# Performance work log

Hardware: AMD Instinct MI355X
Metric: run time of the kernel (lower is better)

## Reference

```python
import jax, jax.numpy as jnp
import numpy as np

N_KERNELS = 11

def _kernel_mus(n):
    l = [1.0]
    bs = 2.0 / (n - 1)
    l.append(1 - bs / 2)
    for i in range(1, n - 1):
        l.append(l[i] - bs)
    return l

def _kernel_sigmas(n):
    bs = 2.0 / (n - 1)
    return [0.001] + [0.5 * bs] * (n - 1)

MU = jnp.asarray(_kernel_mus(N_KERNELS), jnp.float32)      # [K]
SIGMA = jnp.asarray(_kernel_sigmas(N_KERNELS), jnp.float32)  # [K]


def setup_inputs() -> dict:
    key = jax.random.key(0)
    ks = jax.random.split(key, 10)
    V, E, C = 50000, 300, 128
    B, Q, D = 128, 30, 200
    inp = {
        'query_tokens': jax.random.randint(ks[0], (B, Q), 0, V),
        'document_tokens': jax.random.randint(ks[1], (B, D), 0, V),
        'embedding': jax.random.normal(ks[2], (V, E), jnp.float32) * 0.1,
        'conv_w1': jax.random.normal(ks[3], (C, E, 1), jnp.float32) * 0.05,
        'conv_w2': jax.random.normal(ks[4], (C, E, 2), jnp.float32) * 0.05,
        'conv_w3': jax.random.normal(ks[5], (C, E, 3), jnp.float32) * 0.05,
        'conv_b1': jax.random.normal(ks[6], (C,), jnp.float32) * 0.01,
        'conv_b2': jax.random.normal(ks[7], (C,), jnp.float32) * 0.01,
        'conv_b3': jax.random.normal(ks[8], (C,), jnp.float32) * 0.01,
        'dense_w': jax.random.uniform(ks[9], (1, N_KERNELS * 9), jnp.float32, -0.014, 0.014),
    }
    return inp


def _conv_ngram(x_ble, w, b):
    # x_ble: [B, L, E]; w: [C, E, k]; pad (0, k-1) on the length dim -> same length out
    x = x_ble.transpose(0, 2, 1)  # [B, E, L]
    y = jax.lax.conv_general_dilated(
        x, w, window_strides=(1,), padding=[(0, w.shape[2] - 1)],
        dimension_numbers=('NCH', 'OIH', 'NCH'))
    return jax.nn.relu(y + b[None, :, None]).transpose(0, 2, 1)  # [B, L, C]


def _kernel_pool(q, d, qd_mask, q_mask):
    # q: [B,Q,C], d: [B,D,C]; cosine sim -> Gaussian RBF soft-binning -> masked log-sum pooling
    qn = q / (jnp.linalg.norm(q, axis=-1, keepdims=True) + 1e-13)
    dn = d / (jnp.linalg.norm(d, axis=-1, keepdims=True) + 1e-13)
    cos = jnp.einsum('bqc,bdc->bqd', qn, dn) * qd_mask           # [B,Q,D]
    diff = cos[..., None] - MU                                    # [B,Q,D,K]
    kern = jnp.exp(-(diff * diff) / (2.0 * SIGMA * SIGMA)) * qd_mask[..., None]
    per_kernel_query = jnp.sum(kern, axis=2)                      # [B,Q,K]
    logk = jnp.log(jnp.clip(per_kernel_query, 1e-10)) * 0.01
    return jnp.sum(logk * q_mask[..., None], axis=1)              # [B,K]


def reference(query_tokens, document_tokens, embedding,
              conv_w1, conv_w2, conv_w3, conv_b1, conv_b2, conv_b3, dense_w):
    q_mask = (query_tokens > 0).astype(jnp.float32)               # [B,Q]
    d_mask = (document_tokens > 0).astype(jnp.float32)            # [B,D]
    qd_mask = q_mask[:, :, None] * d_mask[:, None, :]             # [B,Q,D]

    q_emb = embedding[query_tokens]                               # [B,Q,E]
    d_emb = embedding[document_tokens]                            # [B,D,E]

    convs = [(conv_w1, conv_b1), (conv_w2, conv_b2), (conv_w3, conv_b3)]
    q_grams = [_conv_ngram(q_emb, w, b) for w, b in convs]
    d_grams = [_conv_ngram(d_emb, w, b) for w, b in convs]

    feats = jnp.concatenate(
        [_kernel_pool(q, d, qd_mask, q_mask) for q in q_grams for d in d_grams],
        axis=1)                                                   # [B, K*9]
    return (feats @ dense_w.T)[:, 0]                              # [B]
```

## Files before the change

### kernel.cpp

```cpp
#include <hip/hip_runtime.h>
#include <hip/hip_bf16.h>
#include <math.h>

#define B_   128
#define Qn   30
#define Dn   200
#define En   300

typedef __attribute__((ext_vector_type(8))) short short8;
typedef __attribute__((ext_vector_type(4))) float floatx4;
typedef unsigned int u32;
typedef unsigned short u16;

static __device__ __forceinline__ u16 f2b(float x) {
    union { float f; u32 u; } v; v.f = x;
    u32 r = v.u + 0x7FFFu + ((v.u >> 16) & 1u);
    return (u16)(r >> 16);
}
static __device__ __forceinline__ float bits2f(u32 u) {
    union { u32 u2; float f; } v; v.u2 = u; return v.f;
}

__global__ void prep_kernel(
    const float* __restrict__ w1, const float* __restrict__ w2, const float* __restrict__ w3,
    u16* __restrict__ Wt3)
{
    int p = (blockIdx.x*128 + blockIdx.y)*256 + threadIdx.x;
    if (p >= 245760) return;
    int ks = p / 24576;
    int r  = p - ks*24576;
    int g, rr;
    if (r < 4096)        { g = 0; rr = r;         }
    else if (r < 12288)  { g = 1; rr = r - 4096;  }
    else                 { g = 2; rr = r - 12288; }
    int j  = rr >> 12;
    int r2 = rr & 4095;
    int nt  = r2 >> 9;
    int q4  = (r2 >> 7) & 3;
    int c16 = (r2 >> 3) & 15;
    int k8  = r2 & 7;
    int ch = nt*16 + c16;
    int e  = ks*32 + q4*8 + k8;
    float v = 0.f;
    if (e < En) {
        if (g == 0)      v = w1[ch*En + e];
        else if (g == 1) v = w2[(ch*En + e)*2 + j];
        else             v = w3[(ch*En + e)*3 + j];
    }
    Wt3[p] = f2b(v);
}

__global__ __launch_bounds__(512, 4) void conv_kernel(
    const int* __restrict__ qtok, const int* __restrict__ dtok,
    const float* __restrict__ emb,
    const u16* __restrict__ Wt3,
    const float* __restrict__ b1, const float* __restrict__ b2, const float* __restrict__ b3,
    u16* __restrict__ qg, u16* __restrict__ dg,
    float* __restrict__ invnq, float* __restrict__ invnd)
{
    __shared__ __align__(16) char smem[43560];
    char* As  = smem;
    int*  toks = (int*)(smem + 43296);

    const int tile = blockIdx.x;
    const int tid = threadIdx.x;
    const int wv = tid >> 6, lane = tid & 63;
    const int l15 = lane & 15, qd4 = lane >> 4;
    const int mh = wv >> 2, nh = wv & 3;
    const int gR0 = tile*64;

    if (tid < 66) {
        int gr = gR0 + tid;
        int t = -1;
        if (gr < 32768) {
            int b = gr >> 8, pos = gr & 255;
            if (pos < Dn) t = dtok[b*Dn + pos];
            else if (pos >= 208 && pos < 238) t = qtok[b*Qn + (pos - 208)];
        }
        toks[tid] = t;
    }
    __syncthreads();

    #pragma unroll
    for (int i = 0; i < 6; ++i) {
        int idx = tid + i*512;
        if (idx < 2640) {
            int r = idx / 40, c4 = idx - r*40;
            int t = toks[r];
            u16 o0=0,o1=0,o2=0,o3=0;
            if (t >= 0) {
                float4 v = *(const float4*)(emb + t*En + c4*4);
                o0=f2b(v.x); o1=f2b(v.y); o2=f2b(v.z); o3=f2b(v.w);
            }
            u16* pdst = (u16*)(As + r*656 + c4*8);
            pdst[0]=o0; pdst[1]=o1; pdst[2]=o2; pdst[3]=o3;
        }
    }

    float bias[3][2];
    #pragma unroll
    for (int nt = 0; nt < 2; ++nt) {
        int ch = nh*32 + nt*16 + l15;
        bias[0][nt] = b1[ch];
        bias[1][nt] = b2[ch];
        bias[2][nt] = b3[ch];
    }

    floatx4 acc[3][2][2];
    #pragma unroll
    for (int g = 0; g < 3; ++g)
        #pragma unroll
        for (int mt = 0; mt < 2; ++mt)
            #pragma unroll
            for (int nt = 0; nt < 2; ++nt)
                acc[g][mt][nt] = (floatx4){0.f,0.f,0.f,0.f};

    __syncthreads();

    float4 hf[6];
    #pragma unroll
    for (int i = 0; i < 6; ++i) {
        int idx = tid + i*512;
        const float* p = emb;
        if (idx < 2640) {
            int r = idx / 40, c = idx - r*40;
            int t = toks[r];
            if (t >= 0 && c < 35) p = emb + t*En + (40 + c)*4;
        }
        hf[i] = *(const float4*)p;
    }

    #pragma unroll 1
    for (int ks = 0; ks < 5; ++ks) {
        short8 af[2][3];
        #pragma unroll
        for (int mt = 0; mt < 2; ++mt)
            #pragma unroll
            for (int j = 0; j < 3; ++j)
                af[mt][j] = *(const short8*)(As + (mh*32 + mt*16 + l15 + j)*656 + ks*64 + qd4*16);
        const u16* Wks = Wt3 + ks*24576;
        #pragma unroll
        for (int g = 0; g < 3; ++g) {
            const int cbW = (g == 0) ? 0 : (g == 1) ? 4096 : 12288;
            #pragma unroll
            for (int j = 0; j <= g; ++j) {
                const u16* bb = Wks + cbW + (j*8 + nh*2)*512 + lane*8;
                short8 w0  = *(const short8*)(bb);
                short8 w1v = *(const short8*)(bb + 512);
                #pragma unroll
                for (int mt = 0; mt < 2; ++mt) {
                    acc[g][mt][0] = __builtin_amdgcn_mfma_f32_16x16x32_bf16(
                        af[mt][j], w0,  acc[g][mt][0], 0, 0, 0);
                    acc[g][mt][1] = __builtin_amdgcn_mfma_f32_16x16x32_bf16(
                        af[mt][j], w1v, acc[g][mt][1], 0, 0, 0);
                }
            }
        }
    }

    #pragma unroll
    for (int i = 0; i < 6; ++i) {
        int idx = tid + i*512;
        if (idx < 2640) {
            int r = idx / 40, c = idx - r*40;
            int t = toks[r];
            bool ok = (t >= 0) && (c < 35);
            u16 o0=0,o1=0,o2=0,o3=0;
            if (ok) { o0=f2b(hf[i].x); o1=f2b(hf[i].y); o2=f2b(hf[i].z); o3=f2b(hf[i].w); }
            u16* pdst = (u16*)(As + r*656 + (40 + c)*8);
            pdst[0]=o0; pdst[1]=o1; pdst[2]=o2; pdst[3]=o3;
        }
    }
    __syncthreads();

    #pragma unroll 1
    for (int ks = 5; ks < 10; ++ks) {
        short8 af[2][3];
        #pragma unroll
        for (int mt = 0; mt < 2; ++mt)
            #pragma unroll
            for (int j = 0; j < 3; ++j)
                af[mt][j] = *(const short8*)(As + (mh*32 + mt*16 + l15 + j)*656 + ks*64 + qd4*16);
        const u16* Wks = Wt3 + ks*24576;
        #pragma unroll
        for (int g = 0; g < 3; ++g) {
            const int cbW = (g == 0) ? 0 : (g == 1) ? 4096 : 12288;
            #pragma unroll
            for (int j = 0; j <= g; ++j) {
                const u16* bb = Wks + cbW + (j*8 + nh*2)*512 + lane*8;
                short8 w0  = *(const short8*)(bb);
                short8 w1v = *(const short8*)(bb + 512);
                #pragma unroll
                for (int mt = 0; mt < 2; ++mt) {
                    acc[g][mt][0] = __builtin_amdgcn_mfma_f32_16x16x32_bf16(
                        af[mt][j], w0,  acc[g][mt][0], 0, 0, 0);
                    acc[g][mt][1] = __builtin_amdgcn_mfma_f32_16x16x32_bf16(
                        af[mt][j], w1v, acc[g][mt][1], 0, 0, 0);
                }
            }
        }
    }

    u16* Gs = (u16*)smem;
    #pragma unroll
    for (int g = 0; g < 3; ++g) {
        __syncthreads();
        #pragma unroll
        for (int mt = 0; mt < 2; ++mt)
            #pragma unroll
            for (int nt = 0; nt < 2; ++nt) {
                int ch = nh*32 + nt*16 + l15;
                #pragma unroll
                for (int i = 0; i < 4; ++i) {
                    int row = mh*32 + mt*16 + qd4*4 + i;
                    Gs[row*136 + ch] = f2b(fmaxf(acc[g][mt][nt][i] + bias[g][nt], 0.f));
                }
            }
        __syncthreads();

        {
            int r = tid >> 3, pp = tid & 7;
            const char* rp = (const char*)Gs + r*272 + pp*32;
            float ssum = 0.f;
            #pragma unroll
            for (int t2 = 0; t2 < 2; ++t2) {
                uint4 u = *(const uint4*)(rp + t2*16);
                float x;
                x = bits2f(u.x << 16); ssum += x*x;  x = bits2f(u.x & 0xffff0000u); ssum += x*x;
                x = bits2f(u.y << 16); ssum += x*x;  x = bits2f(u.y & 0xffff0000u); ssum += x*x;
                x = bits2f(u.z << 16); ssum += x*x;  x = bits2f(u.z & 0xffff0000u); ssum += x*x;
                x = bits2f(u.w << 16); ssum += x*x;  x = bits2f(u.w & 0xffff0000u); ssum += x*x;
            }
            ssum += __shfl_xor(ssum, 1);
            ssum += __shfl_xor(ssum, 2);
            ssum += __shfl_xor(ssum, 4);
            if (pp == 0) {
                float inv = 1.f / (sqrtf(ssum) + 1e-13f);
                int gr = gR0 + r;
                int b = gr >> 8, pos = gr & 255;
                if (pos < 208)      invnd[(g*B_ + b)*208 + pos] = inv;
                else if (pos < 238) invnq[(g*B_ + b)*32 + (pos - 208)] = inv;
            }
        }
        #pragma unroll
        for (int i = 0; i < 2; ++i) {
            int idx = tid + i*512;
            int r = idx >> 4, c16 = idx & 15;
            uint4 v = *(const uint4*)((const char*)Gs + r*272 + c16*16);
            int gr = gR0 + r;
            int b = gr >> 8, pos = gr & 255;
            if (pos < 208)      *(uint4*)(dg + ((g*B_ + b)*208 + pos)*128 + c16*8) = v;
            else if (pos < 238) *(uint4*)(qg + ((g*B_ + b)*32 + (pos - 208))*128 + c16*8) = v;
        }
    }
}

__global__ __launch_bounds__(1024, 2) void pool_kernel(
    const u16* __restrict__ qg, const u16* __restrict__ dg,
    const float* __restrict__ invnq, const float* __restrict__ invnd,
    const int* __restrict__ qtok, const int* __restrict__ dtok,
    float* __restrict__ feats)
{
    __shared__ __align__(16) u16 dsb[208*136];
    __shared__ float pk[96*12];
    __shared__ float invqA[96];
    __shared__ float qmA[96];
    __shared__ __align__(16) float invd[208];

    const int tid = threadIdx.x;
    const int b = blockIdx.y, dj = blockIdx.x;
    const int wv = tid >> 6, lane = tid & 63;
    const int l15 = lane & 15, qd4 = lane >> 4;

    for (int idx = tid; idx < 208*16; idx += 1024) {
        int r = idx >> 4, ch = idx & 15;
        uint4 v = make_uint4(0u,0u,0u,0u);
        if (r < Dn) v = *(const uint4*)(dg + ((dj*B_ + b)*208 + r)*128 + ch*8);
        *(uint4*)((char*)dsb + r*272 + ch*16) = v;
    }
    if (tid < 208) {
        float v = invnd[(dj*B_ + b)*208 + tid];
        bool ok = (tid < Dn) && (dtok[b*Dn + tid] > 0);
        invd[tid] = ok ? v : (-fabsf(v) - 1.0f);
    }
    if (tid < 96) {
        int qi = tid >> 5, qr = tid & 31;
        float v = invnq[(qi*B_ + b)*32 + qr];
        bool ok = (qr < Qn) && (qtok[b*Qn + qr] > 0);
        invqA[tid] = ok ? v : 0.f;
        qmA[tid] = ok ? 1.f : 0.f;
    }
    for (int i = tid; i < 96*12; i += 1024) pk[i] = 0.f;
    __syncthreads();

    const float CkR[9] = {8886110.5f, 162754.79f, 2980.958f, 54.598150f, 1.0f,
                          0.018315639f, 3.3546263e-4f, 6.1442124e-6f, 1.1253517e-7f};

    if (wv < 13) {
        const int t = wv;
        short8 af[4];
        #pragma unroll
        for (int ks = 0; ks < 4; ++ks)
            af[ks] = *(const short8*)((const char*)dsb + (t*16 + l15)*272 + ks*64 + qd4*16);
        floatx4 iv4 = *(const floatx4*)(invd + t*16 + qd4*4);

        #pragma unroll 1
        for (int qi = 0; qi < 3; ++qi) {
            short8 qf[2][4];
            float vq[2];
            #pragma unroll
            for (int qt = 0; qt < 2; ++qt) {
                vq[qt] = invqA[qi*32 + qt*16 + l15];
                #pragma unroll
                for (int ks = 0; ks < 4; ++ks)
                    qf[qt][ks] = *(const short8*)(qg + ((qi*B_ + b)*32 + qt*16 + l15)*128 + ks*32 + qd4*8);
            }
            floatx4 acc[2];
            acc[0] = (floatx4){0.f,0.f,0.f,0.f};
            acc[1] = (floatx4){0.f,0.f,0.f,0.f};
            #pragma unroll
            for (int ks = 0; ks < 4; ++ks)
                #pragma unroll
                for (int qt = 0; qt < 2; ++qt)
                    acc[qt] = __builtin_amdgcn_mfma_f32_16x16x32_bf16(af[ks], qf[qt][ks], acc[qt], 0, 0, 0);

            float pkl[2][11];
            #pragma unroll
            for (int qt = 0; qt < 2; ++qt)
                #pragma unroll
                for (int k = 0; k < 11; ++k) pkl[qt][k] = 0.f;

            #pragma unroll
            for (int qt = 0; qt < 2; ++qt)
                #pragma unroll
                for (int i = 0; i < 4; ++i) {
                    float cs = acc[qt][i] * vq[qt] * iv4[i];
                    cs = (cs > 0.f) ? cs : 2.0f;
                    float t0 = cs - 1.0f;
                    float u  = cs - 0.9f;
                    float s0 = __expf(-500000.f * t0 * t0);
                    float e  = __expf(-50.f * u * u);
                    float rr = __expf(-20.f * cs);
                    pkl[qt][0] += s0;
                    pkl[qt][1] += e;
                    #pragma unroll
                    for (int kk = 0; kk < 9; ++kk) {
                        e = e * rr * CkR[kk];
                        pkl[qt][2 + kk] += e;
                    }
                }
            #pragma unroll
            for (int qt = 0; qt < 2; ++qt)
                #pragma unroll
                for (int k = 0; k < 11; ++k) {
                    float v = pkl[qt][k];
                    v += __shfl_xor(v, 16);
                    v += __shfl_xor(v, 32);
                    if (qd4 == 0) atomicAdd(&pk[(qi*32 + qt*16 + l15)*12 + k], v);
                }
        }
    }
    __syncthreads();

    if (tid < 33) {
        int qi = tid / 11, k = tid - qi*11;
        float s = 0.f;
        for (int q = 0; q < Qn; ++q)
            s += qmA[qi*32 + q] * 0.01f * __logf(fmaxf(pk[(qi*32 + q)*12 + k], 1e-10f));
        feats[(b*9 + qi*3 + dj)*11 + k] = s;
    }
}

__global__ void final_kernel(const float* __restrict__ feats,
                             const float* __restrict__ dw,
                             float* __restrict__ out) {
    int b = threadIdx.x;
    if (b < B_) {
        float s = 0.f;
        for (int f = 0; f < 99; ++f) s += feats[b*99 + f] * dw[f];
        out[b] = s;
    }
}

extern "C" void kernel_launch(void* const* d_in, const int* in_sizes, int n_in,
                              void* d_out, int out_size, void* d_ws, size_t ws_size,
                              hipStream_t stream) {
    const int*   qtok = (const int*)d_in[0];
    const int*   dtok = (const int*)d_in[1];
    const float* emb  = (const float*)d_in[2];
    const float* w1   = (const float*)d_in[3];
    const float* w2   = (const float*)d_in[4];
    const float* w3   = (const float*)d_in[5];
    const float* b1   = (const float*)d_in[6];
    const float* b2   = (const float*)d_in[7];
    const float* b3   = (const float*)d_in[8];
    const float* dw   = (const float*)d_in[9];
    float* out = (float*)d_out;

    char* w = (char*)d_ws;
    u16*   Wt3   = (u16*)w;
    u16*   qg    = (u16*)(w + 491520);
    u16*   dgm   = (u16*)(w + 3637248);
    float* invq_ = (float*)(w + 24084480);
    float* invd_ = (float*)(w + 24133632);
    float* feats = (float*)(w + 24453120);

    prep_kernel<<<dim3(8, B_), 256, 0, stream>>>(w1, w2, w3, Wt3);

    conv_kernel<<<dim3(512), 512, 0, stream>>>(
        qtok, dtok, emb, Wt3, b1, b2, b3, qg, dgm, invq_, invd_);

    pool_kernel<<<dim3(3, B_), 1024, 0, stream>>>(qg, dgm, invq_, invd_, qtok, dtok, feats);

    final_kernel<<<1, 128, 0, stream>>>(feats, dw, out);
}
```

Baseline: 189.9 us.

## Split pool kernel over query n-gram dimension with smaller blocks

Changes the pool kernel grid from (3,B) blocks of 1024 threads into (3,B,3) blocks of 256 threads, with each block handling one query n-gram. Document tiles are now read straight from global memory instead of being staged in LDS, and each wave loops over several document tiles while keeping per-query partial sums in registers. The only atomic reduction into shared memory happens once at the end. This aims to raise occupancy and cut LDS traffic and atomics, but each document tile is now loaded three times from global/L2.

```diff
diff --git a/kernel.cpp b/kernel.cpp
--- a/kernel.cpp
+++ b/kernel.cpp
@@ -255,66 +255,61 @@
     }
 }
 
-__global__ __launch_bounds__(1024, 2) void pool_kernel(
+__global__ __launch_bounds__(256, 4) void pool_kernel(
     const u16* __restrict__ qg, const u16* __restrict__ dg,
     const float* __restrict__ invnq, const float* __restrict__ invnd,
     const int* __restrict__ qtok, const int* __restrict__ dtok,
     float* __restrict__ feats)
 {
-    __shared__ __align__(16) u16 dsb[208*136];
-    __shared__ float pk[96*12];
-    __shared__ float invqA[96];
-    __shared__ float qmA[96];
+    __shared__ float pk[32*12];
+    __shared__ float invqA[32];
+    __shared__ float qmA[32];
     __shared__ __align__(16) float invd[208];
 
     const int tid = threadIdx.x;
-    const int b = blockIdx.y, dj = blockIdx.x;
+    const int b = blockIdx.y, dj = blockIdx.x, qi = blockIdx.z;
     const int wv = tid >> 6, lane = tid & 63;
     const int l15 = lane & 15, qd4 = lane >> 4;
 
-    for (int idx = tid; idx < 208*16; idx += 1024) {
-        int r = idx >> 4, ch = idx & 15;
-        uint4 v = make_uint4(0u,0u,0u,0u);
-        if (r < Dn) v = *(const uint4*)(dg + ((dj*B_ + b)*208 + r)*128 + ch*8);
-        *(uint4*)((char*)dsb + r*272 + ch*16) = v;
-    }
     if (tid < 208) {
         float v = invnd[(dj*B_ + b)*208 + tid];
         bool ok = (tid < Dn) && (dtok[b*Dn + tid] > 0);
         invd[tid] = ok ? v : (-fabsf(v) - 1.0f);
     }
-    if (tid < 96) {
-        int qi = tid >> 5, qr = tid & 31;
-        float v = invnq[(qi*B_ + b)*32 + qr];
-        bool ok = (qr < Qn) && (qtok[b*Qn + qr] > 0);
+    if (tid < 32) {
+        float v = invnq[(qi*B_ + b)*32 + tid];
+        bool ok = (tid < Qn) && (qtok[b*Qn + tid] > 0);
         invqA[tid] = ok ? v : 0.f;
         qmA[tid] = ok ? 1.f : 0.f;
     }
-    for (int i = tid; i < 96*12; i += 1024) pk[i] = 0.f;
+    for (int i = tid; i < 32*12; i += 256) pk[i] = 0.f;
     __syncthreads();
 
     const float CkR[9] = {8886110.5f, 162754.79f, 2980.958f, 54.598150f, 1.0f,
                           0.018315639f, 3.3546263e-4f, 6.1442124e-6f, 1.1253517e-7f};
 
-    if (wv < 13) {
-        const int t = wv;
-        short8 af[4];
-        #pragma unroll
-        for (int ks = 0; ks < 4; ++ks)
-            af[ks] = *(const short8*)((const char*)dsb + (t*16 + l15)*272 + ks*64 + qd4*16);
-        floatx4 iv4 = *(const floatx4*)(invd + t*16 + qd4*4);
-
-        #pragma unroll 1
-        for (int qi = 0; qi < 3; ++qi) {
-            short8 qf[2][4];
-            float vq[2];
-            #pragma unroll
-            for (int qt = 0; qt < 2; ++qt) {
-                vq[qt] = invqA[qi*32 + qt*16 + l15];
-                #pragma unroll
-                for (int ks = 0; ks < 4; ++ks)
-                    qf[qt][ks] = *(const short8*)(qg + ((qi*B_ + b)*32 + qt*16 + l15)*128 + ks*32 + qd4*8);
-            }
+    {
+        short8 qf[2][4];
+        float vq[2];
+        #pragma unroll
+        for (int qt = 0; qt < 2; ++qt) {
+            vq[qt] = invqA[qt*16 + l15];
+            #pragma unroll
+            for (int ks = 0; ks < 4; ++ks)
+                qf[qt][ks] = *(const short8*)(qg + ((qi*B_ + b)*32 + qt*16 + l15)*128 + ks*32 + qd4*8);
+        }
+        float pkl[2][11];
+        #pragma unroll
+        for (int qt = 0; qt < 2; ++qt)
+            #pragma unroll
+            for (int k = 0; k < 11; ++k) pkl[qt][k] = 0.f;
+
+        const u16* dbase = dg + (size_t)(dj*B_ + b)*208*128;
+        for (int t = wv; t < 13; t += 4) {
+            short8 af[4];
+            #pragma unroll
+            for (int ks = 0; ks < 4; ++ks)
+                af[ks] = *(const short8*)(dbase + (t*16 + l15)*128 + ks*32 + qd4*8);
             floatx4 acc[2];
             acc[0] = (floatx4){0.f,0.f,0.f,0.f};
             acc[1] = (floatx4){0.f,0.f,0.f,0.f};
@@ -323,13 +318,7 @@
                 #pragma unroll
                 for (int qt = 0; qt < 2; ++qt)
                     acc[qt] = __builtin_amdgcn_mfma_f32_16x16x32_bf16(af[ks], qf[qt][ks], acc[qt], 0, 0, 0);
-
-            float pkl[2][11];
-            #pragma unroll
-            for (int qt = 0; qt < 2; ++qt)
-                #pragma unroll
-                for (int k = 0; k < 11; ++k) pkl[qt][k] = 0.f;
-
+            floatx4 iv4 = *(const floatx4*)(invd + t*16 + qd4*4);
             #pragma unroll
             for (int qt = 0; qt < 2; ++qt)
                 #pragma unroll
@@ -349,24 +338,24 @@
                         pkl[qt][2 + kk] += e;
                     }
                 }
-            #pragma unroll
-            for (int qt = 0; qt < 2; ++qt)
-                #pragma unroll
-                for (int k = 0; k < 11; ++k) {
-                    float v = pkl[qt][k];
-                    v += __shfl_xor(v, 16);
-                    v += __shfl_xor(v, 32);
-                    if (qd4 == 0) atomicAdd(&pk[(qi*32 + qt*16 + l15)*12 + k], v);
-                }
-        }
+        }
+        #pragma unroll
+        for (int qt = 0; qt < 2; ++qt)
+            #pragma unroll
+            for (int k = 0; k < 11; ++k) {
+                float v = pkl[qt][k];
+                v += __shfl_xor(v, 16);
+                v += __shfl_xor(v, 32);
+                if (qd4 == 0) atomicAdd(&pk[(qt*16 + l15)*12 + k], v);
+            }
     }
     __syncthreads();
 
-    if (tid < 33) {
-        int qi = tid / 11, k = tid - qi*11;
+    if (tid < 11) {
+        int k = tid;
         float s = 0.f;
         for (int q = 0; q < Qn; ++q)
-            s += qmA[qi*32 + q] * 0.01f * __logf(fmaxf(pk[(qi*32 + q)*12 + k], 1e-10f));
+            s += qmA[q] * 0.01f * __logf(fmaxf(pk[q*12 + k], 1e-10f));
         feats[(b*9 + qi*3 + dj)*11 + k] = s;
     }
 }
@@ -410,7 +399,7 @@
     conv_kernel<<<dim3(512), 512, 0, stream>>>(
         qtok, dtok, emb, Wt3, b1, b2, b3, qg, dgm, invq_, invd_);
 
-    pool_kernel<<<dim3(3, B_), 1024, 0, stream>>>(qg, dgm, invq_, invd_, qtok, dtok, feats);
+    pool_kernel<<<dim3(3, B_, 3), 256, 0, stream>>>(qg, dgm, invq_, invd_, qtok, dtok, feats);
 
     final_kernel<<<1, 128, 0, stream>>>(feats, dw, out);
 }
```

Result: faster. 161.6 us (-14.9%).
